# Optimization experiments

Measured on AMD Instinct MI355X. Metric: run time of the kernel, lower is better.

## Reference

```python
import jax, jax.numpy as jnp
import numpy as np

N_NODES = 50000


def setup_inputs() -> dict:
    key = jax.random.key(0)
    k1, k2, k3, k4 = jax.random.split(key, 4)
    N, E, F_IN, F_OUT = N_NODES, 1600000, 512, 128
    x = jax.random.normal(k1, (N, F_IN), dtype=jnp.float32)
    edge_index = jax.random.randint(k2, (2, E), 0, N, dtype=jnp.int64)
    edge_weight = jax.random.uniform(k3, (E,), dtype=jnp.float32)
    # glorot init for weight, zeros bias (as in the original layer)
    limit = np.sqrt(6.0 / (F_IN + F_OUT)).astype(np.float32)
    weight = jax.random.uniform(k4, (F_IN, F_OUT), dtype=jnp.float32,
                                minval=-limit, maxval=limit)
    bias = jnp.zeros((F_OUT,), dtype=jnp.float32)
    return {"x": x, "edge_index": edge_index, "edge_weight": edge_weight,
            "weight": weight, "bias": bias}


def reference(x, edge_index, edge_weight, weight, bias):
    # dropout rate is 0 in this config -> identity
    h = x @ weight                                # [N, F_out] dense transform
    src, dst = edge_index[0], edge_index[1]
    # support @ h : sparse adjacency aggregation (SpMM) via gather + segment_sum
    msgs = h[src] * edge_weight[:, None]          # [E, F_out]
    agg = jax.ops.segment_sum(msgs, dst, num_segments=N_NODES)  # [N, F_out]
    return jax.nn.relu(agg + bias)
```

## Files before the change

### kernel.cpp

```cpp
#include <hip/hip_runtime.h>

#define F_IN  512
#define F_OUT 128
#define CB    128
#define EPB   4096
#define CMAX  512

typedef __attribute__((ext_vector_type(8))) short  short8;
typedef __attribute__((ext_vector_type(4))) float  floatx4;

__device__ __forceinline__ unsigned short f2bf(float f) {
    unsigned u = __float_as_uint(f);
    return (unsigned short)((u + 0x7FFF + ((u >> 16) & 1)) >> 16);
}
__device__ __forceinline__ float bf2f(unsigned b) {
    return __uint_as_float(b << 16);
}

__global__ __launch_bounds__(256) void convert_w(
    const float* __restrict__ w, unsigned short* __restrict__ wt)
{
    int gid = blockIdx.x * 256 + threadIdx.x;
    int n = gid >> 9, k = gid & 511;
    wt[gid] = f2bf(w[(size_t)k * F_OUT + n]);
}

__global__ __launch_bounds__(256, 2) void gemm_mfma(
    const float* __restrict__ x, const unsigned short* __restrict__ wt,
    unsigned short* __restrict__ h, int N)
{
    __shared__ unsigned short sa[64 * 68];
    __shared__ unsigned short sb[128 * 68];

    const int tid  = threadIdx.x;
    const int wave = tid >> 6, lane = tid & 63;
    const int g    = lane >> 4, l16 = lane & 15;
    const int m0   = blockIdx.x * 64;

    const int arow = tid >> 2, aq = tid & 3;
    const int brow = tid >> 1, bh = tid & 1;

    floatx4 acc[8];
    #pragma unroll
    for (int i = 0; i < 8; ++i) acc[i] = (floatx4)(0.f);

    const bool  avalid = (m0 + arow) < N;
    const float* xp = x + (size_t)(m0 + arow) * F_IN + aq * 16;
    const unsigned short* bp = wt + brow * F_IN + bh * 32;

    float4 ax[4];
    uint4  bv[4];
    #pragma unroll
    for (int i = 0; i < 4; ++i) ax[i] = make_float4(0.f, 0.f, 0.f, 0.f);
    if (avalid) {
        #pragma unroll
        for (int i = 0; i < 4; ++i) ax[i] = ((const float4*)xp)[i];
    }
    #pragma unroll
    for (int i = 0; i < 4; ++i) bv[i] = ((const uint4*)bp)[i];

    for (int s = 0; s < 8; ++s) {
        __syncthreads();
        #pragma unroll
        for (int i = 0; i < 4; ++i) {
            ushort4 t;
            t.x = f2bf(ax[i].x); t.y = f2bf(ax[i].y);
            t.z = f2bf(ax[i].z); t.w = f2bf(ax[i].w);
            *(ushort4*)&sa[arow * 68 + aq * 16 + i * 4] = t;
        }
        #pragma unroll
        for (int i = 0; i < 4; ++i) {
            *(uint2*)&sb[brow * 68 + bh * 32 + i * 8]     = make_uint2(bv[i].x, bv[i].y);
            *(uint2*)&sb[brow * 68 + bh * 32 + i * 8 + 4] = make_uint2(bv[i].z, bv[i].w);
        }
        if (s < 7) {
            int k0n = (s + 1) * 64;
            if (avalid) {
                #pragma unroll
                for (int i = 0; i < 4; ++i) ax[i] = ((const float4*)(xp + k0n))[i];
            }
            #pragma unroll
            for (int i = 0; i < 4; ++i) bv[i] = ((const uint4*)(bp + k0n))[i];
        }
        __syncthreads();

        #pragma unroll
        for (int kc = 0; kc < 2; ++kc) {
            union { ushort4 u[2]; short8 v; } af;
            int abase = (wave * 16 + l16) * 68 + kc * 32 + g * 8;
            af.u[0] = *(ushort4*)&sa[abase];
            af.u[1] = *(ushort4*)&sa[abase + 4];
            #pragma unroll
            for (int nt = 0; nt < 8; ++nt) {
                union { ushort4 u[2]; short8 v; } bf;
                int bbase = (nt * 16 + l16) * 68 + kc * 32 + g * 8;
                bf.u[0] = *(ushort4*)&sb[bbase];
                bf.u[1] = *(ushort4*)&sb[bbase + 4];
                acc[nt] = __builtin_amdgcn_mfma_f32_16x16x32_bf16(af.v, bf.v, acc[nt], 0, 0, 0);
            }
        }
    }

    #pragma unroll
    for (int nt = 0; nt < 8; ++nt) {
        #pragma unroll
        for (int r = 0; r < 4; ++r) {
            int row = m0 + wave * 16 + g * 4 + r;
            if (row < N) h[(size_t)row * F_OUT + nt * 16 + l16] = f2bf(acc[nt][r]);
        }
    }
}

__global__ __launch_bounds__(512) void coarse_hist(
    const int* __restrict__ ei, int* __restrict__ cnt, int E, int C)
{
    __shared__ int lh[CMAX];
    int tid = threadIdx.x;
    if (tid < CMAX) lh[tid] = 0;
    __syncthreads();
    int base = blockIdx.x * EPB;
    #pragma unroll
    for (int j = 0; j < EPB / 512; ++j) {
        int e = base + j * 512 + tid;
        if (e < E) atomicAdd(&lh[ei[E + e] >> 7], 1);
    }
    __syncthreads();
    if (tid < C && lh[tid] > 0) atomicAdd(&cnt[tid], lh[tid]);
}

__global__ __launch_bounds__(512) void scan_coarse(
    const int* __restrict__ cnt, int* __restrict__ binoff,
    int* __restrict__ cursor, int* __restrict__ rowptr, int C, int N, int E)
{
    __shared__ int s[CMAX];
    int tid = threadIdx.x;
    int v = (tid < C) ? cnt[tid] : 0;
    s[tid] = v;
    __syncthreads();
    #pragma unroll
    for (int off = 1; off < CMAX; off <<= 1) {
        int t = (tid >= off) ? s[tid - off] : 0;
        __syncthreads();
        s[tid] += t;
        __syncthreads();
    }
    if (tid < C) { int ex = s[tid] - v; binoff[tid] = ex; cursor[tid] = ex; }
    if (tid == 0) { binoff[C] = E; rowptr[N] = E; }
}

__global__ __launch_bounds__(512) void coarse_fill(
    const int* __restrict__ ei, const float* __restrict__ ew,
    int* __restrict__ cursor, unsigned* __restrict__ k32,
    unsigned char* __restrict__ d8, int E, int C)
{
    __shared__ int lh[CMAX];
    __shared__ int lbase[CMAX];
    int tid = threadIdx.x;
    if (tid < CMAX) lh[tid] = 0;
    __syncthreads();

    const int base = blockIdx.x * EPB;
    unsigned      mykey[EPB / 512];
    unsigned char mydl[EPB / 512];
    short         mybin[EPB / 512];
    unsigned short myrank[EPB / 512];

    #pragma unroll
    for (int j = 0; j < EPB / 512; ++j) {
        int e = base + j * 512 + tid;
        mybin[j] = -1;
        if (e < E) {
            int   src = ei[e];
            int   dst = ei[E + e];
            float w   = ew[e];
            int bin = dst >> 7;
            mykey[j]  = (unsigned)src | ((unsigned)f2bf(w) << 16);
            mydl[j]   = (unsigned char)(dst & (CB - 1));
            mybin[j]  = (short)bin;
            myrank[j] = (unsigned short)atomicAdd(&lh[bin], 1);
        }
    }
    __syncthreads();
    if (tid < C && lh[tid] > 0) lbase[tid] = atomicAdd(&cursor[tid], lh[tid]);
    __syncthreads();
    #pragma unroll
    for (int j = 0; j < EPB / 512; ++j) {
        if (mybin[j] >= 0) {
            int p = lbase[mybin[j]] + myrank[j];
            k32[p] = mykey[j];
            d8[p]  = mydl[j];
        }
    }
}

__global__ __launch_bounds__(512) void fine_fill(
    const unsigned* __restrict__ k32, const unsigned char* __restrict__ d8,
    const int* __restrict__ binoff, unsigned* __restrict__ bucket,
    int* __restrict__ rowptr, int N)
{
    __shared__ int lh[CB];
    __shared__ int ss[CB];
    __shared__ int lcur[CB];

    const int b   = blockIdx.x;
    const int tid = threadIdx.x;
    const int start = binoff[b];
    const int end   = binoff[b + 1];

    if (tid < CB) lh[tid] = 0;
    __syncthreads();
    for (int i = start + tid; i < end; i += 512)
        atomicAdd(&lh[d8[i]], 1);
    __syncthreads();

    if (tid < CB) ss[tid] = lh[tid];
    __syncthreads();
    #pragma unroll
    for (int off = 1; off < CB; off <<= 1) {
        int t = 0;
        if (tid < CB && tid >= off) t = ss[tid - off];
        __syncthreads();
        if (tid < CB) ss[tid] += t;
        __syncthreads();
    }
    if (tid < CB) {
        int ex = ss[tid] - lh[tid];
        lcur[tid] = ex;
        int node = b * CB + tid;
        if (node < N) rowptr[node] = start + ex;
    }
    __syncthreads();

    for (int i = start + tid; i < end; i += 512) {
        int nd = d8[i];
        int r  = atomicAdd(&lcur[nd], 1);
        bucket[start + r] = k32[i];
    }
}

__global__ __launch_bounds__(256) void aggregate_csr(
    const unsigned short* __restrict__ h, const unsigned* __restrict__ bucket,
    const int* __restrict__ rowptr, const float* __restrict__ bias,
    float* __restrict__ out, int N)
{
    int wave = threadIdx.x >> 6;
    int lane = threadIdx.x & 63;
    int n    = blockIdx.x * 4 + wave;
    if (n >= N) return;

    int start = rowptr[n];
    int end   = rowptr[n + 1];

    float accx = 0.f, accy = 0.f;
    int i = start;
    for (; i + 4 <= end; i += 4) {
        unsigned b0 = bucket[i], b1 = bucket[i + 1], b2 = bucket[i + 2], b3 = bucket[i + 3];
        unsigned h0 = *(const unsigned*)&h[(size_t)(b0 & 0xFFFF) * F_OUT + lane * 2];
        unsigned h1 = *(const unsigned*)&h[(size_t)(b1 & 0xFFFF) * F_OUT + lane * 2];
        unsigned h2 = *(const unsigned*)&h[(size_t)(b2 & 0xFFFF) * F_OUT + lane * 2];
        unsigned h3 = *(const unsigned*)&h[(size_t)(b3 & 0xFFFF) * F_OUT + lane * 2];
        float w0 = bf2f(b0 >> 16), w1 = bf2f(b1 >> 16);
        float w2 = bf2f(b2 >> 16), w3 = bf2f(b3 >> 16);
        accx += bf2f(h0 & 0xFFFF) * w0; accy += bf2f(h0 >> 16) * w0;
        accx += bf2f(h1 & 0xFFFF) * w1; accy += bf2f(h1 >> 16) * w1;
        accx += bf2f(h2 & 0xFFFF) * w2; accy += bf2f(h2 >> 16) * w2;
        accx += bf2f(h3 & 0xFFFF) * w3; accy += bf2f(h3 >> 16) * w3;
    }
    for (; i < end; ++i) {
        unsigned b  = bucket[i];
        unsigned hv = *(const unsigned*)&h[(size_t)(b & 0xFFFF) * F_OUT + lane * 2];
        float wgt = bf2f(b >> 16);
        accx += bf2f(hv & 0xFFFF) * wgt;
        accy += bf2f(hv >> 16) * wgt;
    }

    float2 bv = *(const float2*)&bias[lane * 2];
    float2 o;
    o.x = fmaxf(accx + bv.x, 0.f);
    o.y = fmaxf(accy + bv.y, 0.f);
    *(float2*)&out[(size_t)n * F_OUT + lane * 2] = o;
}

static inline size_t align256(size_t x) { return (x + 255) & ~(size_t)255; }

extern "C" void kernel_launch(void* const* d_in, const int* in_sizes, int n_in,
                              void* d_out, int out_size, void* d_ws, size_t ws_size,
                              hipStream_t stream)
{
    const float* x    = (const float*)d_in[0];
    const int*   ei   = (const int*)  d_in[1];
    const float* ew   = (const float*)d_in[2];
    const float* w    = (const float*)d_in[3];
    const float* bias = (const float*)d_in[4];
    float*       out  = (float*)d_out;

    const int N = in_sizes[0] / F_IN;
    const int E = in_sizes[2];
    const int C = (N + CB - 1) / CB;

    char*  ws = (char*)d_ws;
    size_t off = 0;
    unsigned short* h      = (unsigned short*)(ws + off); off += align256((size_t)N * F_OUT * 2);
    unsigned short* wt     = (unsigned short*)(ws + off); off += align256((size_t)F_OUT * F_IN * 2);
    int*            cnt    = (int*)(ws + off);            off += align256((size_t)(C + 1) * 4);
    int*            binoff = (int*)(ws + off);            off += align256((size_t)(C + 1) * 4);
    int*            cursor = (int*)(ws + off);            off += align256((size_t)C * 4);
    int*            rowptr = (int*)(ws + off);            off += align256((size_t)(N + 1) * 4);
    unsigned*       k32    = (unsigned*)(ws + off);       off += align256((size_t)E * 4);
    unsigned char*  d8     = (unsigned char*)(ws + off);  off += align256((size_t)E);
    unsigned*       bucket = (unsigned*)(ws + off);       off += align256((size_t)E * 4);

    const int pblocks = (E + EPB - 1) / EPB;

    (void)hipMemsetAsync(cnt, 0, (size_t)C * 4, stream);
    coarse_hist<<<pblocks, 512, 0, stream>>>(ei, cnt, E, C);
    scan_coarse<<<1, 512, 0, stream>>>(cnt, binoff, cursor, rowptr, C, N, E);
    coarse_fill<<<pblocks, 512, 0, stream>>>(ei, ew, cursor, k32, d8, E, C);
    fine_fill<<<C, 512, 0, stream>>>(k32, d8, binoff, bucket, rowptr, N);

    convert_w<<<(F_IN * F_OUT) / 256, 256, 0, stream>>>(w, wt);
    gemm_mfma<<<(N + 63) / 64, 256, 0, stream>>>(x, wt, h, N);

    aggregate_csr<<<(N + 3) / 4, 256, 0, stream>>>(h, bucket, rowptr, bias, out, N);
}
```

Measured before the change: 299.0 us.

## Fuse fine bucket sort into aggregation via shared-memory sort per coarse bin

```diff
diff --git a/kernel.cpp b/kernel.cpp
--- a/kernel.cpp
+++ b/kernel.cpp
@@ -5,6 +5,7 @@
 #define CB    128
 #define EPB   4096
 #define CMAX  512
+#define CAP   8192
 
 typedef __attribute__((ext_vector_type(8))) short  short8;
 typedef __attribute__((ext_vector_type(4))) float  floatx4;
@@ -15,14 +16,6 @@
 }
 __device__ __forceinline__ float bf2f(unsigned b) {
     return __uint_as_float(b << 16);
-}
-
-__global__ __launch_bounds__(256) void convert_w(
-    const float* __restrict__ w, unsigned short* __restrict__ wt)
-{
-    int gid = blockIdx.x * 256 + threadIdx.x;
-    int n = gid >> 9, k = gid & 511;
-    wt[gid] = f2bf(w[(size_t)k * F_OUT + n]);
 }
 
 __global__ __launch_bounds__(256, 2) void gemm_mfma(
@@ -128,10 +121,17 @@
     if (tid < C && lh[tid] > 0) atomicAdd(&cnt[tid], lh[tid]);
 }
 
-__global__ __launch_bounds__(512) void scan_coarse(
+__global__ __launch_bounds__(512) void scan_convert(
     const int* __restrict__ cnt, int* __restrict__ binoff,
-    int* __restrict__ cursor, int* __restrict__ rowptr, int C, int N, int E)
-{
+    int* __restrict__ cursor, int C, int E,
+    const float* __restrict__ w, unsigned short* __restrict__ wt)
+{
+    if (blockIdx.x > 0) {
+        int gid = (blockIdx.x - 1) * 512 + threadIdx.x;
+        int n = gid >> 9, k = gid & 511;
+        wt[gid] = f2bf(w[(size_t)k * F_OUT + n]);
+        return;
+    }
     __shared__ int s[CMAX];
     int tid = threadIdx.x;
     int v = (tid < C) ? cnt[tid] : 0;
@@ -145,7 +145,7 @@
         __syncthreads();
     }
     if (tid < C) { int ex = s[tid] - v; binoff[tid] = ex; cursor[tid] = ex; }
-    if (tid == 0) { binoff[C] = E; rowptr[N] = E; }
+    if (tid == 0) binoff[C] = E;
 }
 
 __global__ __launch_bounds__(512) void coarse_fill(
@@ -160,9 +160,9 @@
     __syncthreads();
 
     const int base = blockIdx.x * EPB;
-    unsigned      mykey[EPB / 512];
-    unsigned char mydl[EPB / 512];
-    short         mybin[EPB / 512];
+    unsigned       mykey[EPB / 512];
+    unsigned char  mydl[EPB / 512];
+    short          mybin[EPB / 512];
     unsigned short myrank[EPB / 512];
 
     #pragma unroll
@@ -193,92 +193,119 @@
     }
 }
 
-__global__ __launch_bounds__(512) void fine_fill(
-    const unsigned* __restrict__ k32, const unsigned char* __restrict__ d8,
-    const int* __restrict__ binoff, unsigned* __restrict__ bucket,
-    int* __restrict__ rowptr, int N)
-{
-    __shared__ int lh[CB];
-    __shared__ int ss[CB];
-    __shared__ int lcur[CB];
-
-    const int b   = blockIdx.x;
-    const int tid = threadIdx.x;
+__global__ __launch_bounds__(512) void fine_agg(
+    const unsigned short* __restrict__ h, const unsigned* __restrict__ k32,
+    const unsigned char* __restrict__ d8, const int* __restrict__ binoff,
+    const float* __restrict__ bias, float* __restrict__ out, int N)
+{
+    __shared__ unsigned char sd[CAP];
+    __shared__ unsigned      ssort[CAP];
+    __shared__ int lh[CB], ssum[CB], lcur[CB];
+    __shared__ int sso[CB + 1];
+
+    const int b     = blockIdx.x;
+    const int tid   = threadIdx.x;
     const int start = binoff[b];
-    const int end   = binoff[b + 1];
-
-    if (tid < CB) lh[tid] = 0;
-    __syncthreads();
-    for (int i = start + tid; i < end; i += 512)
-        atomicAdd(&lh[d8[i]], 1);
-    __syncthreads();
-
-    if (tid < CB) ss[tid] = lh[tid];
-    __syncthreads();
-    #pragma unroll
-    for (int off = 1; off < CB; off <<= 1) {
-        int t = 0;
-        if (tid < CB && tid >= off) t = ss[tid - off];
-        __syncthreads();
-        if (tid < CB) ss[tid] += t;
-        __syncthreads();
-    }
-    if (tid < CB) {
-        int ex = ss[tid] - lh[tid];
-        lcur[tid] = ex;
-        int node = b * CB + tid;
-        if (node < N) rowptr[node] = start + ex;
-    }
-    __syncthreads();
-
-    for (int i = start + tid; i < end; i += 512) {
-        int nd = d8[i];
-        int r  = atomicAdd(&lcur[nd], 1);
-        bucket[start + r] = k32[i];
-    }
-}
-
-__global__ __launch_bounds__(256) void aggregate_csr(
-    const unsigned short* __restrict__ h, const unsigned* __restrict__ bucket,
-    const int* __restrict__ rowptr, const float* __restrict__ bias,
-    float* __restrict__ out, int N)
-{
-    int wave = threadIdx.x >> 6;
-    int lane = threadIdx.x & 63;
-    int n    = blockIdx.x * 4 + wave;
-    if (n >= N) return;
-
-    int start = rowptr[n];
-    int end   = rowptr[n + 1];
-
-    float accx = 0.f, accy = 0.f;
-    int i = start;
-    for (; i + 4 <= end; i += 4) {
-        unsigned b0 = bucket[i], b1 = bucket[i + 1], b2 = bucket[i + 2], b3 = bucket[i + 3];
-        unsigned h0 = *(const unsigned*)&h[(size_t)(b0 & 0xFFFF) * F_OUT + lane * 2];
-        unsigned h1 = *(const unsigned*)&h[(size_t)(b1 & 0xFFFF) * F_OUT + lane * 2];
-        unsigned h2 = *(const unsigned*)&h[(size_t)(b2 & 0xFFFF) * F_OUT + lane * 2];
-        unsigned h3 = *(const unsigned*)&h[(size_t)(b3 & 0xFFFF) * F_OUT + lane * 2];
-        float w0 = bf2f(b0 >> 16), w1 = bf2f(b1 >> 16);
-        float w2 = bf2f(b2 >> 16), w3 = bf2f(b3 >> 16);
-        accx += bf2f(h0 & 0xFFFF) * w0; accy += bf2f(h0 >> 16) * w0;
-        accx += bf2f(h1 & 0xFFFF) * w1; accy += bf2f(h1 >> 16) * w1;
-        accx += bf2f(h2 & 0xFFFF) * w2; accy += bf2f(h2 >> 16) * w2;
-        accx += bf2f(h3 & 0xFFFF) * w3; accy += bf2f(h3 >> 16) * w3;
-    }
-    for (; i < end; ++i) {
-        unsigned b  = bucket[i];
-        unsigned hv = *(const unsigned*)&h[(size_t)(b & 0xFFFF) * F_OUT + lane * 2];
-        float wgt = bf2f(b >> 16);
-        accx += bf2f(hv & 0xFFFF) * wgt;
-        accy += bf2f(hv >> 16) * wgt;
-    }
-
-    float2 bv = *(const float2*)&bias[lane * 2];
-    float2 o;
-    o.x = fmaxf(accx + bv.x, 0.f);
-    o.y = fmaxf(accy + bv.y, 0.f);
-    *(float2*)&out[(size_t)n * F_OUT + lane * 2] = o;
+    const int cnt   = binoff[b + 1] - start;
+    const int wave  = tid >> 6;
+    const int lane  = tid & 63;
+    const int half  = lane >> 5;
+    const int q     = lane & 31;
+    const float4 bv = *(const float4*)&bias[q * 4];
+
+    if (cnt <= CAP) {
+        if (tid < CB) lh[tid] = 0;
+        __syncthreads();
+        for (int i = tid; i < cnt; i += 512) {
+            unsigned char d = d8[start + i];
+            sd[i] = d;
+            atomicAdd(&lh[d], 1);
+        }
+        __syncthreads();
+        if (tid < CB) ssum[tid] = lh[tid];
+        __syncthreads();
+        #pragma unroll
+        for (int off = 1; off < CB; off <<= 1) {
+            int t = 0;
+            if (tid < CB && tid >= off) t = ssum[tid - off];
+            __syncthreads();
+            if (tid < CB) ssum[tid] += t;
+            __syncthreads();
+        }
+        if (tid < CB) {
+            int ex = ssum[tid] - lh[tid];
+            sso[tid]  = ex;
+            lcur[tid] = ex;
+        }
+        if (tid == 0) sso[CB] = cnt;
+        __syncthreads();
+        for (int i = tid; i < cnt; i += 512) {
+            unsigned k = k32[start + i];
+            int r = atomicAdd(&lcur[sd[i]], 1);
+            ssort[r] = k;
+        }
+        __syncthreads();
+
+        #pragma unroll 1
+        for (int t = 0; t < 16; ++t) {
+            int nd   = wave * 16 + t;
+            int node = b * CB + nd;
+            int s    = sso[nd], e = sso[nd + 1];
+            float4 acc = make_float4(0.f, 0.f, 0.f, 0.f);
+            for (int i = s; i < e; i += 8) {
+                #pragma unroll
+                for (int j = 0; j < 4; ++j) {
+                    int idx = i + j * 2 + half;
+                    unsigned bk = 0;
+                    if (idx < e) bk = ssort[idx];
+                    float wgt = bf2f(bk >> 16);
+                    uint2 hv = *(const uint2*)&h[(size_t)(bk & 0xFFFF) * F_OUT + q * 4];
+                    acc.x += bf2f(hv.x & 0xFFFF) * wgt;
+                    acc.y += bf2f(hv.x >> 16)    * wgt;
+                    acc.z += bf2f(hv.y & 0xFFFF) * wgt;
+                    acc.w += bf2f(hv.y >> 16)    * wgt;
+                }
+            }
+            acc.x += __shfl_xor(acc.x, 32);
+            acc.y += __shfl_xor(acc.y, 32);
+            acc.z += __shfl_xor(acc.z, 32);
+            acc.w += __shfl_xor(acc.w, 32);
+            if (half == 0 && node < N) {
+                float4 o;
+                o.x = fmaxf(acc.x + bv.x, 0.f);
+                o.y = fmaxf(acc.y + bv.y, 0.f);
+                o.z = fmaxf(acc.z + bv.z, 0.f);
+                o.w = fmaxf(acc.w + bv.w, 0.f);
+                *(float4*)&out[(size_t)node * F_OUT + q * 4] = o;
+            }
+        }
+    } else {
+        #pragma unroll 1
+        for (int t = 0; t < 16; ++t) {
+            int nd   = wave * 16 + t;
+            int node = b * CB + nd;
+            float4 acc = make_float4(0.f, 0.f, 0.f, 0.f);
+            for (int i = 0; i < cnt; ++i) {
+                if (d8[start + i] == (unsigned char)nd) {
+                    unsigned bk = k32[start + i];
+                    float wgt = bf2f(bk >> 16);
+                    uint2 hv = *(const uint2*)&h[(size_t)(bk & 0xFFFF) * F_OUT + q * 4];
+                    acc.x += bf2f(hv.x & 0xFFFF) * wgt;
+                    acc.y += bf2f(hv.x >> 16)    * wgt;
+                    acc.z += bf2f(hv.y & 0xFFFF) * wgt;
+                    acc.w += bf2f(hv.y >> 16)    * wgt;
+                }
+            }
+            if (half == 0 && node < N) {
+                float4 o;
+                o.x = fmaxf(acc.x + bv.x, 0.f);
+                o.y = fmaxf(acc.y + bv.y, 0.f);
+                o.z = fmaxf(acc.z + bv.z, 0.f);
+                o.w = fmaxf(acc.w + bv.w, 0.f);
+                *(float4*)&out[(size_t)node * F_OUT + q * 4] = o;
+            }
+        }
+    }
 }
 
 static inline size_t align256(size_t x) { return (x + 255) & ~(size_t)255; }
@@ -305,21 +332,15 @@
     int*            cnt    = (int*)(ws + off);            off += align256((size_t)(C + 1) * 4);
     int*            binoff = (int*)(ws + off);            off += align256((size_t)(C + 1) * 4);
     int*            cursor = (int*)(ws + off);            off += align256((size_t)C * 4);
-    int*            rowptr = (int*)(ws + off);            off += align256((size_t)(N + 1) * 4);
     unsigned*       k32    = (unsigned*)(ws + off);       off += align256((size_t)E * 4);
     unsigned char*  d8     = (unsigned char*)(ws + off);  off += align256((size_t)E);
-    unsigned*       bucket = (unsigned*)(ws + off);       off += align256((size_t)E * 4);
 
     const int pblocks = (E + EPB - 1) / EPB;
 
     (void)hipMemsetAsync(cnt, 0, (size_t)C * 4, stream);
     coarse_hist<<<pblocks, 512, 0, stream>>>(ei, cnt, E, C);
-    scan_coarse<<<1, 512, 0, stream>>>(cnt, binoff, cursor, rowptr, C, N, E);
+    scan_convert<<<1 + (F_IN * F_OUT) / 512, 512, 0, stream>>>(cnt, binoff, cursor, C, E, w, wt);
     coarse_fill<<<pblocks, 512, 0, stream>>>(ei, ew, cursor, k32, d8, E, C);
-    fine_fill<<<C, 512, 0, stream>>>(k32, d8, binoff, bucket, rowptr, N);
-
-    convert_w<<<(F_IN * F_OUT) / 256, 256, 0, stream>>>(w, wt);
     gemm_mfma<<<(N + 63) / 64, 256, 0, stream>>>(x, wt, h, N);
-
-    aggregate_csr<<<(N + 3) / 4, 256, 0, stream>>>(h, bucket, rowptr, bias, out, N);
-}
+    fine_agg<<<C, 512, 0, stream>>>(h, k32, d8, binoff, bias, out, N);
+}
```

After: 280.9 us. 6.0% less time.
